# Optimization experiments

Hardware: AMD Instinct MI355X
Metric: run time of the kernel (lower is better)

The kernel has to match this reference:

```python
import jax, jax.numpy as jnp
import numpy as np

IMAGE_SIZE = 224
EPS = 1e-8


def _minmax_global(x, eps=EPS):
    # torch normalize_minmax: global min-max over the whole tensor,
    # returning zeros if the range is degenerate.
    lo = x.min()
    hi = x.max()
    y = (x - lo) / (hi - lo + eps)
    return jnp.where(hi - lo < eps, jnp.zeros_like(x), y)


def setup_inputs() -> dict:
    key = jax.random.key(0)
    x = jax.random.normal(key, (16, 1024, 8), dtype=jnp.float32)  # [B, L, D]
    return {"x": x}


def reference(x):
    B, L, D = x.shape
    # --- gramian_angular_field ---
    x_norm = _minmax_global(x) * 2.0 - 1.0                      # [B, L, D]
    theta = jnp.arccos(jnp.clip(x_norm, -1.0 + 1e-6, 1.0 - 1e-6))
    th = jnp.transpose(theta, (0, 2, 1))                        # [B, D, L]
    # fused batched pairwise cos-sum (replaces B*D python-loop kernels)
    cos_sum = jnp.cos(th[:, :, :, None] + th[:, :, None, :])    # [B, D, L, L]
    # per-(b,d) min-max normalization in one pass
    lo = cos_sum.min(axis=(2, 3), keepdims=True)
    hi = cos_sum.max(axis=(2, 3), keepdims=True)
    gaf = jnp.where(hi - lo < EPS,
                    jnp.zeros_like(cos_sum),
                    (cos_sum - lo) / (hi - lo + EPS))
    gaf = gaf.mean(axis=1, keepdims=True)                       # [B, 1, L, L]
    # bilinear resize, align_corners=False (half-pixel centers)
    gaf = jax.image.resize(gaf, (B, 1, IMAGE_SIZE, IMAGE_SIZE),
                           method="linear", antialias=False)
    gaf = jnp.repeat(gaf, 3, axis=1)                            # RGB (grayscale=False)
    # --- final norm(): global shift/scale ---
    out = gaf - gaf.min()
    out = out / (out.max() + 1e-6)
    return out
```

## Files before the change

### kernel.cpp

```cpp
#include <hip/hip_runtime.h>
#include <math.h>

#define B_ 16
#define L_ 1024
#define IMG 224
#define PIX (IMG*IMG)
#define NBD 128

#define OFF_A     0
#define OFF_TERM  128
#define OFF_GPMIN 256
#define OFF_GPMAX 768
#define OFF_T     1280
#define OFF_G     58624

__device__ __forceinline__ float cclip(float xn) {
    return fminf(fmaxf(xn, -1.0f + 1e-6f), 1.0f - 1e-6f);
}
__device__ __forceinline__ int bucketf(float c) {
    int k = (int)((c + 1.0f) * 512.0f);
    return min(1023, max(0, k));
}

template <int NTHR>
__device__ __forceinline__ void block_minmax_share(float mn, float mx, float* red) {
    #pragma unroll
    for (int off = 32; off > 0; off >>= 1) {
        mn = fminf(mn, __shfl_down(mn, off));
        mx = fmaxf(mx, __shfl_down(mx, off));
    }
    const int lane = threadIdx.x & 63;
    const int wave = threadIdx.x >> 6;
    if (lane == 0) { red[2 + wave*2] = mn; red[3 + wave*2] = mx; }
    __syncthreads();
    if (threadIdx.x == 0) {
        #pragma unroll
        for (int w = 1; w < NTHR/64; ++w) {
            mn = fminf(mn, red[2 + w*2]);
            mx = fmaxf(mx, red[3 + w*2]);
        }
        red[0] = mn; red[1] = mx;
    }
    __syncthreads();
}

__global__ __launch_bounds__(512) void k_bd(const float* __restrict__ x,
                                            float* __restrict__ wsf) {
    __shared__ float red[20];
    __shared__ float corig[L_];
    __shared__ float arr[L_];
    __shared__ int   cnt[1024];
    __shared__ int   pref[1025];
    const int bd = blockIdx.x;
    const int b = bd >> 3, d = bd & 7;
    const int t = threadIdx.x;

    float mn = 1e30f, mx = -1e30f;
    const float4* xv = (const float4*)x;
    #pragma unroll 4
    for (int i = t; i < 32768; i += 512) {
        float4 v = xv[i];
        mn = fminf(mn, fminf(fminf(v.x, v.y), fminf(v.z, v.w)));
        mx = fmaxf(mx, fmaxf(fmaxf(v.x, v.y), fmaxf(v.z, v.w)));
    }
    block_minmax_share<512>(mn, mx, red);
    float lo = red[0], hi = red[1], r = hi - lo, sc, sh;
    if (r < 1e-8f) { sc = 0.0f; sh = -1.0f; }
    else           { sc = 2.0f / (r + 1e-8f); sh = -lo*sc - 1.0f; }

    cnt[t] = 0; cnt[t + 512] = 0;
    float cmn = 1e30f, cmx = -1e30f;
    #pragma unroll
    for (int k = 0; k < 2; ++k) {
        int i = t + k*512;
        float c = cclip(x[((size_t)(b*L_ + i))*8 + d]*sc + sh);
        corig[i] = c;
        cmn = fminf(cmn, c); cmx = fmaxf(cmx, c);
    }
    block_minmax_share<512>(cmn, cmx, red);
    float cMin = red[0], cMax = red[1];

    #pragma unroll
    for (int k = 0; k < 2; ++k)
        atomicAdd(&cnt[bucketf(corig[t + k*512])], 1);
    __syncthreads();
    if (t < 64) {
        int s = 0;
        #pragma unroll
        for (int e = 0; e < 16; ++e) s += cnt[t*16 + e];
        int v = s;
        #pragma unroll
        for (int o = 1; o < 64; o <<= 1) {
            int u = __shfl_up(v, o);
            if (t >= o) v += u;
        }
        int run = v - s;
        #pragma unroll
        for (int e = 0; e < 16; ++e) { pref[t*16 + e] = run; run += cnt[t*16 + e]; }
        if (t == 63) pref[L_] = run;
    }
    __syncthreads();
    cnt[t] = pref[t]; cnt[t + 512] = pref[t + 512];
    __syncthreads();
    #pragma unroll
    for (int k = 0; k < 2; ++k) {
        float c = corig[t + k*512];
        int p = atomicAdd(&cnt[bucketf(c)], 1);
        arr[p] = c;
    }
    __syncthreads();

    float rowmin = 1e30f;
    #pragma unroll
    for (int k = 0; k < 2; ++k) {
        float ci = corig[t + k*512];
        float si = sqrtf(fmaxf(1.0f - ci*ci, 0.0f));
        int kt = bucketf(-ci);
        int lo_p = pref[kt], hi_p = pref[kt + 1];
        int start = lo_p, end = hi_p;
        if (lo_p > 0)   start = pref[bucketf(arr[lo_p - 1])];
        if (hi_p < L_)  end   = pref[bucketf(arr[hi_p]) + 1];
        for (int p = start; p < end; ++p) {
            float cj = arr[p];
            float sj = sqrtf(fmaxf(1.0f - cj*cj, 0.0f));
            rowmin = fminf(rowmin, ci*cj - si*sj);
        }
    }
    block_minmax_share<512>(rowmin, -1e30f, red);
    if (t == 0) {
        float plo = red[0];
        float phi = fmaxf(2.0f*cMin*cMin - 1.0f, 2.0f*cMax*cMax - 1.0f);
        float rr  = phi - plo;
        float inv = (rr < 1e-8f) ? 0.0f : 1.0f / (rr + 1e-8f);
        wsf[OFF_A + bd]    = inv * 0.125f;
        wsf[OFF_TERM + bd] = plo * inv * 0.125f;
    }

    if (t < IMG) {
        const float SC = 1024.0f / 224.0f;
        float syf = (t + 0.5f)*SC - 0.5f;
        int i0 = (int)floorf(syf);
        i0 = max(0, min(i0, L_ - 2));
        float f = syf - (float)i0;
        float ca = corig[i0], cb = corig[i0 + 1];
        float sa = sqrtf(fmaxf(1.0f - ca*ca, 0.0f));
        float sb = sqrtf(fmaxf(1.0f - cb*cb, 0.0f));
        size_t base = OFF_T + ((size_t)(b*IMG + t))*16;
        wsf[base + d]     = ca + f*(cb - ca);
        wsf[base + 8 + d] = sa + f*(sb - sa);
    }
}

__global__ __launch_bounds__(256) void k_resize(float* __restrict__ wsf) {
    __shared__ float lds_y[112];
    __shared__ float red[16];
    int b     = blockIdx.x >> 5;
    int strip = blockIdx.x & 31;
    const float* tb = wsf + OFF_T + (size_t)b*IMG*16;
    int t = threadIdx.x;
    if (t < 112) lds_y[t] = tb[strip*112 + t];
    __syncthreads();
    int ox = min(t, IMG-1);
    bool active = (t < IMG);
    const float4* xt = (const float4*)(tb + (size_t)ox*16);
    float4 cx0 = xt[0], cx1 = xt[1], sx0 = xt[2], sx1 = xt[3];
    const float4* av = (const float4*)(wsf + OFF_A + b*8);
    float4 a0 = av[0], a1 = av[1];
    float bias = 0.f;
    #pragma unroll
    for (int dd = 0; dd < 8; ++dd) bias += wsf[OFF_TERM + b*8 + dd];
    float mn = 1e30f, mx = -1e30f;
    #pragma unroll
    for (int rr = 0; rr < 7; ++rr) {
        const float* Y = lds_y + rr*16;
        float acc;
        acc  = (a0.x*Y[0])*cx0.x - (a0.x*Y[ 8])*sx0.x;
        acc += (a0.y*Y[1])*cx0.y - (a0.y*Y[ 9])*sx0.y;
        acc += (a0.z*Y[2])*cx0.z - (a0.z*Y[10])*sx0.z;
        acc += (a0.w*Y[3])*cx0.w - (a0.w*Y[11])*sx0.w;
        acc += (a1.x*Y[4])*cx1.x - (a1.x*Y[12])*sx1.x;
        acc += (a1.y*Y[5])*cx1.y - (a1.y*Y[13])*sx1.y;
        acc += (a1.z*Y[6])*cx1.z - (a1.z*Y[14])*sx1.z;
        acc += (a1.w*Y[7])*cx1.w - (a1.w*Y[15])*sx1.w;
        float g = acc - bias;
        if (active) {
            int oy = strip*7 + rr;
            wsf[OFF_G + ((size_t)(b*IMG + oy))*IMG + ox] = g;
            mn = fminf(mn, g);
            mx = fmaxf(mx, g);
        }
    }
    block_minmax_share<256>(mn, mx, red);
    if (t == 0) {
        wsf[OFF_GPMIN + blockIdx.x] = red[0];
        wsf[OFF_GPMAX + blockIdx.x] = red[1];
    }
}

__global__ __launch_bounds__(256) void k_out(const float* __restrict__ wsf,
                                             float* __restrict__ out) {
    __shared__ float red[16];
    int t = threadIdx.x;
    float pmn = fminf(wsf[OFF_GPMIN + t], wsf[OFF_GPMIN + t + 256]);
    float pmx = fmaxf(wsf[OFF_GPMAX + t], wsf[OFF_GPMAX + t + 256]);
    block_minmax_share<256>(pmn, pmx, red);
    float gmin = red[0];
    float scale = 1.0f / ((red[1] - gmin) + 1e-6f);
    int idx = blockIdx.x*256 + t;
    float4 gv = ((const float4*)(wsf + OFF_G))[idx];
    float4 v;
    v.x = (gv.x - gmin)*scale;
    v.y = (gv.y - gmin)*scale;
    v.z = (gv.z - gmin)*scale;
    v.w = (gv.w - gmin)*scale;
    int b   = idx / (PIX/4);
    int rem = idx - b*(PIX/4);
    float4* ob = (float4*)(out + (size_t)b*3*PIX) + rem;
    ob[0]         = v;
    ob[PIX/4]     = v;
    ob[2*(PIX/4)] = v;
}

extern "C" void kernel_launch(void* const* d_in, const int* in_sizes, int n_in,
                              void* d_out, int out_size, void* d_ws, size_t ws_size,
                              hipStream_t stream) {
    const float* x = (const float*)d_in[0];
    float* out     = (float*)d_out;
    float* wsf     = (float*)d_ws;

    k_bd    <<<NBD,            512, 0, stream>>>(x, wsf);
    k_resize<<<512,            256, 0, stream>>>(wsf);
    k_out   <<<(B_*PIX/4)/256, 256, 0, stream>>>(wsf, out);
}
```

Before: 28.20 us.

## Fuse per-(b,d) stats and resize into one per-batch-half kernel

Merges the per-(b,d) statistics kernel and the resize kernel into a single kernel with 32 blocks of 1024 threads. Each block handles one batch and one half of the output rows, processing all 8 channels together with per-channel histograms in LDS. The resize becomes a shared-memory rank-16 dot product that reuses precomputed scaled row and column vectors, which removes one launch and the workspace round trip. In exchange the grid shrinks from 128+512 blocks to 32, so GPU occupancy is much lower and the per-(b,d) work is computed twice (once per half), which risks making the front stage slower.

New measurement: 58.75 us. +108.4%, slower.

```diff
diff --git a/kernel.cpp b/kernel.cpp
--- a/kernel.cpp
+++ b/kernel.cpp
@@ -5,14 +5,10 @@
 #define L_ 1024
 #define IMG 224
 #define PIX (IMG*IMG)
-#define NBD 128
-
-#define OFF_A     0
-#define OFF_TERM  128
-#define OFF_GPMIN 256
-#define OFF_GPMAX 768
-#define OFF_T     1280
-#define OFF_G     58624
+
+#define OFF_GPMIN 0
+#define OFF_GPMAX 32
+#define OFF_G     64
 
 __device__ __forceinline__ float cclip(float xn) {
     return fminf(fmaxf(xn, -1.0f + 1e-6f), 1.0f - 1e-6f);
@@ -44,165 +40,230 @@
     __syncthreads();
 }
 
-__global__ __launch_bounds__(512) void k_bd(const float* __restrict__ x,
-                                            float* __restrict__ wsf) {
-    __shared__ float red[20];
-    __shared__ float corig[L_];
-    __shared__ float arr[L_];
-    __shared__ int   cnt[1024];
-    __shared__ int   pref[1025];
-    const int bd = blockIdx.x;
-    const int b = bd >> 3, d = bd & 7;
+__device__ __forceinline__ void perd_minmax(float mn, float mx,
+                                            float* scratch,
+                                            float* outmn, float* outmx) {
+    #pragma unroll
+    for (int o = 8; o <= 32; o <<= 1) {
+        mn = fminf(mn, __shfl_xor(mn, o));
+        mx = fmaxf(mx, __shfl_xor(mx, o));
+    }
+    int lane = threadIdx.x & 63, w = threadIdx.x >> 6;
+    if (lane < 8) { scratch[(w*8 + lane)*2] = mn; scratch[(w*8 + lane)*2 + 1] = mx; }
+    __syncthreads();
+    if (threadIdx.x < 8) {
+        float m = 1e30f, M = -1e30f;
+        #pragma unroll
+        for (int ww = 0; ww < 16; ++ww) {
+            m = fminf(m, scratch[(ww*8 + threadIdx.x)*2]);
+            M = fmaxf(M, scratch[(ww*8 + threadIdx.x)*2 + 1]);
+        }
+        outmn[threadIdx.x] = m; outmx[threadIdx.x] = M;
+    }
+    __syncthreads();
+}
+
+__global__ __launch_bounds__(1024) void k_bd_fused(const float* __restrict__ x,
+                                                   float* __restrict__ wsf) {
+    __shared__ float red[34];
+    __shared__ __align__(16) float corig[L_*8];
+    __shared__ __align__(16) float arr[8][L_];
+    __shared__ __align__(16) unsigned char ubuf[8*1024*4 + 8*1026*2];
+    __shared__ float pdred[256];
+    __shared__ float cdmn[8], cdmx[8], aLds[8], termLds[8];
+    __shared__ float biasLds;
+
+    int* cnt            = (int*)ubuf;
+    unsigned short* prf = (unsigned short*)(ubuf + 32768);
+    float* PQ           = (float*)ubuf;
+
+    const int blk = blockIdx.x;
+    const int b = blk >> 1, h = blk & 1;
     const int t = threadIdx.x;
-
-    float mn = 1e30f, mx = -1e30f;
-    const float4* xv = (const float4*)x;
-    #pragma unroll 4
-    for (int i = t; i < 32768; i += 512) {
-        float4 v = xv[i];
-        mn = fminf(mn, fminf(fminf(v.x, v.y), fminf(v.z, v.w)));
-        mx = fmaxf(mx, fmaxf(fmaxf(v.x, v.y), fmaxf(v.z, v.w)));
-    }
-    block_minmax_share<512>(mn, mx, red);
+    const int d = t & 7;
+
+#define CNT(dd,k)  cnt[(dd)*1024 + (k)]
+#define PREF(dd,k) prf[(dd)*1026 + (k)]
+
+    {
+        float mn = 1e30f, mx = -1e30f;
+        const float4* xv = (const float4*)x;
+        #pragma unroll 4
+        for (int i = t; i < 32768; i += 1024) {
+            float4 v = xv[i];
+            mn = fminf(mn, fminf(fminf(v.x, v.y), fminf(v.z, v.w)));
+            mx = fmaxf(mx, fmaxf(fmaxf(v.x, v.y), fmaxf(v.z, v.w)));
+        }
+        block_minmax_share<1024>(mn, mx, red);
+    }
     float lo = red[0], hi = red[1], r = hi - lo, sc, sh;
     if (r < 1e-8f) { sc = 0.0f; sh = -1.0f; }
     else           { sc = 2.0f / (r + 1e-8f); sh = -lo*sc - 1.0f; }
 
-    cnt[t] = 0; cnt[t + 512] = 0;
-    float cmn = 1e30f, cmx = -1e30f;
-    #pragma unroll
-    for (int k = 0; k < 2; ++k) {
-        int i = t + k*512;
-        float c = cclip(x[((size_t)(b*L_ + i))*8 + d]*sc + sh);
-        corig[i] = c;
-        cmn = fminf(cmn, c); cmx = fmaxf(cmx, c);
-    }
-    block_minmax_share<512>(cmn, cmx, red);
-    float cMin = red[0], cMax = red[1];
-
-    #pragma unroll
-    for (int k = 0; k < 2; ++k)
-        atomicAdd(&cnt[bucketf(corig[t + k*512])], 1);
-    __syncthreads();
-    if (t < 64) {
-        int s = 0;
-        #pragma unroll
-        for (int e = 0; e < 16; ++e) s += cnt[t*16 + e];
-        int v = s;
-        #pragma unroll
-        for (int o = 1; o < 64; o <<= 1) {
-            int u = __shfl_up(v, o);
-            if (t >= o) v += u;
-        }
-        int run = v - s;
-        #pragma unroll
-        for (int e = 0; e < 16; ++e) { pref[t*16 + e] = run; run += cnt[t*16 + e]; }
-        if (t == 63) pref[L_] = run;
-    }
-    __syncthreads();
-    cnt[t] = pref[t]; cnt[t + 512] = pref[t + 512];
-    __syncthreads();
-    #pragma unroll
-    for (int k = 0; k < 2; ++k) {
-        float c = corig[t + k*512];
-        int p = atomicAdd(&cnt[bucketf(c)], 1);
-        arr[p] = c;
-    }
-    __syncthreads();
-
-    float rowmin = 1e30f;
-    #pragma unroll
-    for (int k = 0; k < 2; ++k) {
-        float ci = corig[t + k*512];
-        float si = sqrtf(fmaxf(1.0f - ci*ci, 0.0f));
-        int kt = bucketf(-ci);
-        int lo_p = pref[kt], hi_p = pref[kt + 1];
-        int start = lo_p, end = hi_p;
-        if (lo_p > 0)   start = pref[bucketf(arr[lo_p - 1])];
-        if (hi_p < L_)  end   = pref[bucketf(arr[hi_p]) + 1];
-        for (int p = start; p < end; ++p) {
-            float cj = arr[p];
-            float sj = sqrtf(fmaxf(1.0f - cj*cj, 0.0f));
-            rowmin = fminf(rowmin, ci*cj - si*sj);
-        }
-    }
-    block_minmax_share<512>(rowmin, -1e30f, red);
-    if (t == 0) {
-        float plo = red[0];
-        float phi = fmaxf(2.0f*cMin*cMin - 1.0f, 2.0f*cMax*cMax - 1.0f);
+    float c[8];
+    {
+        const float* xb = x + (size_t)b*8192;
+        float cmn = 1e30f, cmx = -1e30f;
+        #pragma unroll
+        for (int k = 0; k < 8; ++k) {
+            int e = t + k*1024;
+            float cv = cclip(xb[e]*sc + sh);
+            c[k] = cv;
+            corig[e] = cv;
+            cnt[e] = 0;
+            cmn = fminf(cmn, cv); cmx = fmaxf(cmx, cv);
+        }
+        __syncthreads();
+        perd_minmax(cmn, cmx, pdred, cdmn, cdmx);
+    }
+
+    #pragma unroll
+    for (int k = 0; k < 8; ++k)
+        atomicAdd(&CNT(d, bucketf(c[k])), 1);
+    __syncthreads();
+
+    {
+        int w = t >> 6, lane = t & 63;
+        if (w < 8) {
+            int s = 0;
+            #pragma unroll
+            for (int e = 0; e < 16; ++e) s += CNT(w, lane*16 + e);
+            int v = s;
+            #pragma unroll
+            for (int o = 1; o < 64; o <<= 1) {
+                int u = __shfl_up(v, o);
+                if (lane >= o) v += u;
+            }
+            int run = v - s;
+            #pragma unroll
+            for (int e = 0; e < 16; ++e) {
+                PREF(w, lane*16 + e) = (unsigned short)run;
+                run += CNT(w, lane*16 + e);
+            }
+            if (lane == 63) PREF(w, 1024) = (unsigned short)run;
+        }
+    }
+    __syncthreads();
+    #pragma unroll
+    for (int k = 0; k < 8; ++k) {
+        int idx = t + k*1024;
+        cnt[idx] = (int)PREF(idx >> 10, idx & 1023);
+    }
+    __syncthreads();
+    #pragma unroll
+    for (int k = 0; k < 8; ++k) {
+        int p = atomicAdd(&CNT(d, bucketf(c[k])), 1);
+        arr[d][p] = c[k];
+    }
+    __syncthreads();
+
+    {
+        float rowmin = 1e30f;
+        const float* arrd = &arr[d][0];
+        #pragma unroll
+        for (int k = 0; k < 8; ++k) {
+            float ci = c[k];
+            float si = sqrtf(fmaxf(1.0f - ci*ci, 0.0f));
+            int kt = bucketf(-ci);
+            int lo_p = (int)PREF(d, kt), hi_p = (int)PREF(d, kt + 1);
+            int start = lo_p, end = hi_p;
+            if (lo_p > 0)    start = (int)PREF(d, bucketf(arrd[lo_p - 1]));
+            if (hi_p < L_)   end   = (int)PREF(d, bucketf(arrd[hi_p]) + 1);
+            for (int p = start; p < end; ++p) {
+                float cj = arrd[p];
+                float sj = sqrtf(fmaxf(1.0f - cj*cj, 0.0f));
+                rowmin = fminf(rowmin, ci*cj - si*sj);
+            }
+        }
+        __syncthreads();
+        perd_minmax(rowmin, -1e30f, pdred, aLds , termLds );
+    }
+    if (t < 8) {
+        float plo = aLds[t];
+        float cm = cdmn[t], cM = cdmx[t];
+        float phi = fmaxf(2.0f*cm*cm - 1.0f, 2.0f*cM*cM - 1.0f);
         float rr  = phi - plo;
         float inv = (rr < 1e-8f) ? 0.0f : 1.0f / (rr + 1e-8f);
-        wsf[OFF_A + bd]    = inv * 0.125f;
-        wsf[OFF_TERM + bd] = plo * inv * 0.125f;
-    }
-
-    if (t < IMG) {
+        aLds[t]    = inv * 0.125f;
+        termLds[t] = plo * inv * 0.125f;
+    }
+    __syncthreads();
+    if (t == 0) {
+        float s = 0.f;
+        #pragma unroll
+        for (int dd = 0; dd < 8; ++dd) s += termLds[dd];
+        biasLds = s;
+    }
+    __syncthreads();
+
+    for (int e = t; e < 1792; e += 1024) {
+        int o = e >> 3, dd = e & 7;
         const float SC = 1024.0f / 224.0f;
-        float syf = (t + 0.5f)*SC - 0.5f;
+        float syf = (o + 0.5f)*SC - 0.5f;
         int i0 = (int)floorf(syf);
         i0 = max(0, min(i0, L_ - 2));
         float f = syf - (float)i0;
-        float ca = corig[i0], cb = corig[i0 + 1];
+        float ca = corig[i0*8 + dd], cb = corig[(i0+1)*8 + dd];
         float sa = sqrtf(fmaxf(1.0f - ca*ca, 0.0f));
         float sb = sqrtf(fmaxf(1.0f - cb*cb, 0.0f));
-        size_t base = OFF_T + ((size_t)(b*IMG + t))*16;
-        wsf[base + d]     = ca + f*(cb - ca);
-        wsf[base + 8 + d] = sa + f*(sb - sa);
-    }
-}
-
-__global__ __launch_bounds__(256) void k_resize(float* __restrict__ wsf) {
-    __shared__ float lds_y[112];
-    __shared__ float red[16];
-    int b     = blockIdx.x >> 5;
-    int strip = blockIdx.x & 31;
-    const float* tb = wsf + OFF_T + (size_t)b*IMG*16;
-    int t = threadIdx.x;
-    if (t < 112) lds_y[t] = tb[strip*112 + t];
-    __syncthreads();
-    int ox = min(t, IMG-1);
-    bool active = (t < IMG);
-    const float4* xt = (const float4*)(tb + (size_t)ox*16);
-    float4 cx0 = xt[0], cx1 = xt[1], sx0 = xt[2], sx1 = xt[3];
-    const float4* av = (const float4*)(wsf + OFF_A + b*8);
-    float4 a0 = av[0], a1 = av[1];
-    float bias = 0.f;
-    #pragma unroll
-    for (int dd = 0; dd < 8; ++dd) bias += wsf[OFF_TERM + b*8 + dd];
-    float mn = 1e30f, mx = -1e30f;
-    #pragma unroll
-    for (int rr = 0; rr < 7; ++rr) {
-        const float* Y = lds_y + rr*16;
-        float acc;
-        acc  = (a0.x*Y[0])*cx0.x - (a0.x*Y[ 8])*sx0.x;
-        acc += (a0.y*Y[1])*cx0.y - (a0.y*Y[ 9])*sx0.y;
-        acc += (a0.z*Y[2])*cx0.z - (a0.z*Y[10])*sx0.z;
-        acc += (a0.w*Y[3])*cx0.w - (a0.w*Y[11])*sx0.w;
-        acc += (a1.x*Y[4])*cx1.x - (a1.x*Y[12])*sx1.x;
-        acc += (a1.y*Y[5])*cx1.y - (a1.y*Y[13])*sx1.y;
-        acc += (a1.z*Y[6])*cx1.z - (a1.z*Y[14])*sx1.z;
-        acc += (a1.w*Y[7])*cx1.w - (a1.w*Y[15])*sx1.w;
-        float g = acc - bias;
-        if (active) {
-            int oy = strip*7 + rr;
-            wsf[OFF_G + ((size_t)(b*IMG + oy))*IMG + ox] = g;
-            mn = fminf(mn, g);
-            mx = fmaxf(mx, g);
-        }
-    }
-    block_minmax_share<256>(mn, mx, red);
-    if (t == 0) {
-        wsf[OFF_GPMIN + blockIdx.x] = red[0];
-        wsf[OFF_GPMAX + blockIdx.x] = red[1];
-    }
+        float hc = ca + f*(cb - ca);
+        float hs = sa + f*(sb - sa);
+        float ad = aLds[dd];
+        PQ[o*20 + dd]            = ad * hc;
+        PQ[o*20 + 8 + dd]        = ad * hs;
+        PQ[4480 + o*20 + dd]     = hc;
+        PQ[4480 + o*20 + 8 + dd] = -hs;
+    }
+    __syncthreads();
+
+    {
+        int ty = t >> 6, tx = t & 63;
+        bool act = (tx < 56);
+        int txc = act ? tx : 0;
+        float4 Xq[4][4];
+        #pragma unroll
+        for (int j = 0; j < 4; ++j) {
+            const float4* qv = (const float4*)&PQ[4480 + (txc + 56*j)*20];
+            Xq[j][0] = qv[0]; Xq[j][1] = qv[1]; Xq[j][2] = qv[2]; Xq[j][3] = qv[3];
+        }
+        float bias = biasLds;
+        float mn = 1e30f, mx = -1e30f;
+        #pragma unroll
+        for (int rr = 0; rr < 7; ++rr) {
+            int oy = h*112 + ty*7 + rr;
+            const float4* yv = (const float4*)&PQ[oy*20];
+            float4 Y0 = yv[0], Y1 = yv[1], Y2 = yv[2], Y3 = yv[3];
+            #pragma unroll
+            for (int j = 0; j < 4; ++j) {
+                float acc;
+                acc  = Y0.x*Xq[j][0].x + Y0.y*Xq[j][0].y + Y0.z*Xq[j][0].z + Y0.w*Xq[j][0].w;
+                acc += Y1.x*Xq[j][1].x + Y1.y*Xq[j][1].y + Y1.z*Xq[j][1].z + Y1.w*Xq[j][1].w;
+                acc += Y2.x*Xq[j][2].x + Y2.y*Xq[j][2].y + Y2.z*Xq[j][2].z + Y2.w*Xq[j][2].w;
+                acc += Y3.x*Xq[j][3].x + Y3.y*Xq[j][3].y + Y3.z*Xq[j][3].z + Y3.w*Xq[j][3].w;
+                float g = acc - bias;
+                if (act) {
+                    wsf[OFF_G + (size_t)b*PIX + (size_t)oy*IMG + tx + 56*j] = g;
+                    mn = fminf(mn, g);
+                    mx = fmaxf(mx, g);
+                }
+            }
+        }
+        block_minmax_share<1024>(mn, mx, red);
+        if (t == 0) {
+            wsf[OFF_GPMIN + blk] = red[0];
+            wsf[OFF_GPMAX + blk] = red[1];
+        }
+    }
+#undef CNT
+#undef PREF
 }
 
 __global__ __launch_bounds__(256) void k_out(const float* __restrict__ wsf,
                                              float* __restrict__ out) {
     __shared__ float red[16];
     int t = threadIdx.x;
-    float pmn = fminf(wsf[OFF_GPMIN + t], wsf[OFF_GPMIN + t + 256]);
-    float pmx = fmaxf(wsf[OFF_GPMAX + t], wsf[OFF_GPMAX + t + 256]);
+    float pmn = (t < 32) ? wsf[OFF_GPMIN + t] :  1e30f;
+    float pmx = (t < 32) ? wsf[OFF_GPMAX + t] : -1e30f;
     block_minmax_share<256>(pmn, pmx, red);
     float gmin = red[0];
     float scale = 1.0f / ((red[1] - gmin) + 1e-6f);
@@ -228,7 +289,6 @@
     float* out     = (float*)d_out;
     float* wsf     = (float*)d_ws;
 
-    k_bd    <<<NBD,            512, 0, stream>>>(x, wsf);
-    k_resize<<<512,            256, 0, stream>>>(wsf);
-    k_out   <<<(B_*PIX/4)/256, 256, 0, stream>>>(wsf, out);
-}
+    k_bd_fused<<<32,             1024, 0, stream>>>(x, wsf);
+    k_out     <<<(B_*PIX/4)/256, 256,  0, stream>>>(wsf, out);
+}
```
